# Kernel optimization log

Hardware: AMD Instinct MI355X
Metric: run time of the kernel (lower is better)

Reference implementation:

```python
import jax, jax.numpy as jnp
import numpy as np

DIM = 2048
NUM_HEADS = 16
HEAD_DIM = DIM // NUM_HEADS
HIDDEN = 4 * DIM
EPS = 1e-6


def rmsnorm(x, w):
    # Faithful to source: weight * (x * dim**-0.5 / sqrt(mean(x^2) + eps))
    scale = DIM ** -0.5
    norm = jnp.sqrt(jnp.mean(x * x, axis=-1, keepdims=True) + EPS)
    return w * (x * scale / norm)


def setup_inputs() -> dict:
    key = jax.random.key(0)
    ks = jax.random.split(key, 10)
    def init(k, shape, fan_in):
        return jax.random.normal(k, shape, dtype=jnp.float32) * (fan_in ** -0.5)
    return {
        "x": jax.random.normal(ks[0], (2, 2048, DIM), dtype=jnp.float32),
        "norm1_w": jnp.ones((DIM,), dtype=jnp.float32),
        "wq": init(ks[1], (DIM, DIM), DIM),
        "wk": init(ks[2], (HEAD_DIM, DIM), DIM),
        "wv": init(ks[3], (HEAD_DIM, DIM), DIM),
        "wo": init(ks[4], (DIM, DIM), DIM),
        "norm2_w": jnp.ones((DIM,), dtype=jnp.float32),
        "w1": init(ks[5], (HIDDEN, DIM), DIM),
        "w2": init(ks[6], (DIM, HIDDEN), HIDDEN),
        "w3": init(ks[7], (HIDDEN, DIM), DIM),
    }


def reference(x, norm1_w, wq, wk, wv, wo, norm2_w, w1, w2, w3):
    B, S, _ = x.shape
    # --- Multi-Query Attention (pre-norm) ---
    h = rmsnorm(x, norm1_w)
    q = h @ wq.T                                  # [B,S,D]
    k = h @ wk.T                                  # [B,S,hd] (shared across heads)
    v = h @ wv.T                                  # [B,S,hd]
    q = q.reshape(B, S, NUM_HEADS, HEAD_DIM)
    # scores: q @ k^T / sqrt(hd); k is broadcast (repeated) across heads
    scores = jnp.einsum('bshd,btd->bhst', q, k) / (HEAD_DIM ** 0.5)  # [B,H,S,S]
    probs = jax.nn.softmax(scores, axis=-1)
    attn = jnp.einsum('bhst,btd->bshd', probs, v).reshape(B, S, DIM)
    x = x + attn @ wo.T
    # --- SwiGLU FFN (pre-norm) ---
    h = rmsnorm(x, norm2_w)
    ffn = (jax.nn.silu(h @ w1.T) * (h @ w3.T)) @ w2.T
    return x + ffn
```

## Files before the change

kernel.cpp:

```cpp
#include <hip/hip_runtime.h>
#include <hip/hip_bf16.h>

typedef __attribute__((ext_vector_type(4))) float f32x4;
typedef __attribute__((ext_vector_type(8))) short s16x8;
typedef __attribute__((ext_vector_type(4))) short s16x4;
typedef __attribute__((ext_vector_type(2))) short s16x2;

#define MFMA_BF16 __builtin_amdgcn_mfma_f32_16x16x32_bf16

__device__ inline short f2bf(float f) {
  unsigned u = __float_as_uint(f);
  u = (u + 0x7FFFu + ((u >> 16) & 1u)) >> 16;
  return (short)u;
}
__device__ inline float bf2f(short s) {
  return __uint_as_float(((unsigned)(unsigned short)s) << 16);
}

#define DPPF(x, ctrl) __int_as_float(__builtin_amdgcn_update_dpp( \
    __float_as_int(x), __float_as_int(x), ctrl, 0xF, 0xF, false))
__device__ inline float rowmax16(float x) {
  x = fmaxf(x, DPPF(x, 0xB1));
  x = fmaxf(x, DPPF(x, 0x4E));
  x = fmaxf(x, DPPF(x, 0x124));
  x = fmaxf(x, DPPF(x, 0x128));
  return x;
}
__device__ inline float rowsum16(float x) {
  x += DPPF(x, 0xB1);
  x += DPPF(x, 0x4E);
  x += DPPF(x, 0x124);
  x += DPPF(x, 0x128);
  return x;
}

__device__ inline void supertile_map(int gx, int gy, int& bx, int& by) {
  int orig = blockIdx.y * gx + blockIdx.x;
  int x   = orig & 7;
  int lin = orig >> 3;
  int sw  = gx >> 3;
  int bg  = lin / (sw * 8);
  int rem = lin % (sw * 8);
  bx = x * sw + (rem >> 3);
  by = bg * 8 + (rem & 7);
}

__global__ __launch_bounds__(256) void cvt_kernel(
    const float* __restrict__ in, short* __restrict__ out, int n, float scale)
{
  int idx = (blockIdx.x * 256 + threadIdx.x) * 8;
  if (idx >= n) return;
  f32x4 a = *(const f32x4*)(in + idx);
  f32x4 b = *(const f32x4*)(in + idx + 4);
  s16x8 o;
  #pragma unroll
  for (int j = 0; j < 4; ++j) { o[j] = f2bf(a[j] * scale); o[4 + j] = f2bf(b[j] * scale); }
  *(s16x8*)(out + idx) = o;
}

__global__ __launch_bounds__(256) void rmsnorm_kernel(
    const float* __restrict__ x, const float* __restrict__ w, short* __restrict__ out)
{
  size_t row = blockIdx.x;
  const float* xr = x + row * 2048;
  int base = threadIdx.x * 8;
  f32x4 a = *(const f32x4*)(xr + base);
  f32x4 b = *(const f32x4*)(xr + base + 4);
  float ss = a[0]*a[0] + a[1]*a[1] + a[2]*a[2] + a[3]*a[3]
           + b[0]*b[0] + b[1]*b[1] + b[2]*b[2] + b[3]*b[3];
  #pragma unroll
  for (int off = 1; off < 64; off <<= 1) ss += __shfl_xor(ss, off, 64);
  __shared__ float red[4];
  if ((threadIdx.x & 63) == 0) red[threadIdx.x >> 6] = ss;
  __syncthreads();
  float tot = red[0] + red[1] + red[2] + red[3];
  float rn = rsqrtf(tot * (1.0f / 2048.0f) + 1e-6f) * 0.022097086912079608f;
  f32x4 wa = *(const f32x4*)(w + base);
  f32x4 wb = *(const f32x4*)(w + base + 4);
  s16x8 o;
  #pragma unroll
  for (int j = 0; j < 4; ++j) {
    o[j]     = f2bf(a[j] * wa[j] * rn);
    o[4 + j] = f2bf(b[j] * wb[j] * rn);
  }
  *(s16x8*)(out + row * 2048 + base) = o;
}

template <int MODE>
__global__ __launch_bounds__(256, 2) void gemm_bt_kernel(
    const short* __restrict__ A, const short* __restrict__ B,
    void* __restrict__ Cv, const float* __restrict__ resid,
    int M, int N, int K)
{
  __shared__ short As[128 * 32];
  __shared__ short Bs[128 * 32];
  int tid = threadIdx.x;
  int lane = tid & 63;
  int w = tid >> 6;
  int r = lane & 15, g = lane >> 4;
  int wr = w >> 1, wc = w & 1;
  size_t row0 = (size_t)blockIdx.y * 128;
  size_t col0 = (size_t)blockIdx.x * 128;

  f32x4 acc[4][4];
  #pragma unroll
  for (int i = 0; i < 4; ++i)
    #pragma unroll
    for (int j = 0; j < 4; ++j) acc[i][j] = (f32x4){0.f, 0.f, 0.f, 0.f};

  const short* Ablk = A + row0 * K;
  const short* Bblk = B + col0 * K;
  int arow = tid >> 2;
  int akk = (tid & 3) << 3;

  for (int k0 = 0; k0 < K; k0 += 32) {
    #pragma unroll
    for (int i = 0; i < 2; ++i) {
      int chunk = i * 256 + tid;
      int rr = i * 64 + arow;
      __builtin_amdgcn_global_load_lds(
          (const __attribute__((address_space(1))) unsigned int*)(Ablk + (size_t)rr * K + k0 + akk),
          (__attribute__((address_space(3))) unsigned int*)(&As[chunk * 8]), 16, 0, 0);
      __builtin_amdgcn_global_load_lds(
          (const __attribute__((address_space(1))) unsigned int*)(Bblk + (size_t)rr * K + k0 + akk),
          (__attribute__((address_space(3))) unsigned int*)(&Bs[chunk * 8]), 16, 0, 0);
    }
    __syncthreads();
    s16x8 af[4], bfr[4];
    #pragma unroll
    for (int mm = 0; mm < 4; ++mm)
      af[mm] = *(const s16x8*)(&As[(wr * 64 + mm * 16 + r) * 32 + g * 8]);
    #pragma unroll
    for (int nn = 0; nn < 4; ++nn)
      bfr[nn] = *(const s16x8*)(&Bs[(wc * 64 + nn * 16 + r) * 32 + g * 8]);
    #pragma unroll
    for (int mm = 0; mm < 4; ++mm)
      #pragma unroll
      for (int nn = 0; nn < 4; ++nn)
        acc[mm][nn] = MFMA_BF16(af[mm], bfr[nn], acc[mm][nn], 0, 0, 0);
    __syncthreads();
  }

  #pragma unroll
  for (int mm = 0; mm < 4; ++mm) {
    #pragma unroll
    for (int nn = 0; nn < 4; ++nn) {
      #pragma unroll
      for (int j = 0; j < 4; ++j) {
        size_t rr = row0 + wr * 64 + mm * 16 + g * 4 + j;
        size_t cc = col0 + wc * 64 + nn * 16 + r;
        size_t idx = rr * (size_t)N + cc;
        if constexpr (MODE == 0) {
          ((short*)Cv)[idx] = f2bf(acc[mm][nn][j]);
        } else {
          ((float*)Cv)[idx] = acc[mm][nn][j] + resid[idx];
        }
      }
    }
  }
}

#define STAGEA1(T)                                                             \
  _Pragma("unroll")                                                            \
  for (int i = 0; i < 4; ++i) {                                                \
    int lc = i * 256 + tid;                                                    \
    int rw = lc >> 3, ch = lc & 7;                                             \
    __builtin_amdgcn_global_load_lds(                                          \
        (const __attribute__((address_space(1))) unsigned int*)                \
            (Ablk + (size_t)rw * K + (T) * 64 + ((ch ^ (rw & 7)) << 3)),       \
        (__attribute__((address_space(3))) unsigned int*)                      \
            (&As[(T) & 1][lc * 8]), 16, 0, 0);                                 \
  }

#define STAGEB1(T)                                                             \
  _Pragma("unroll")                                                            \
  for (int i = 0; i < 4; ++i) {                                                \
    int lc = i * 256 + tid;                                                    \
    int rw = lc >> 3, ch = lc & 7;                                             \
    __builtin_amdgcn_global_load_lds(                                          \
        (const __attribute__((address_space(1))) unsigned int*)                \
            (Bblk + (size_t)rw * K + (T) * 64 + ((ch ^ (rw & 7)) << 3)),       \
        (__attribute__((address_space(3))) unsigned int*)                      \
            (&Bs[(T) & 1][lc * 8]), 16, 0, 0);                                 \
  }

#define LDK(KS, D)                                                             \
  _Pragma("unroll")                                                            \
  for (int mi = 0; mi < 4; ++mi) {                                             \
    int rowa = wr * 64 + mi * 16 + r;                                          \
    aR[mi] = *(const s16x8*)(&As[D][rowa * 64 + (((KS) * 4 + g) ^ (rowa & 7)) * 8]); \
  }                                                                            \
  _Pragma("unroll")                                                            \
  for (int ni = 0; ni < 4; ++ni) {                                             \
    int rowb = wc * 64 + ni * 16 + r;                                          \
    bR[ni] = *(const s16x8*)(&Bs[D][rowb * 64 + (((KS) * 4 + g) ^ (rowb & 7)) * 8]); \
  }

#define MF16A                                                                  \
  __builtin_amdgcn_s_setprio(1);                                               \
  _Pragma("unroll")                                                            \
  for (int mi = 0; mi < 4; ++mi)                                               \
    _Pragma("unroll")                                                          \
    for (int ni = 0; ni < 4; ++ni)                                             \
      acc[mi][ni] = MFMA_BF16(aR[mi], bR[ni], acc[mi][ni], 0, 0, 0);           \
  __builtin_amdgcn_s_setprio(0);

#define BAR __builtin_amdgcn_s_barrier()

template <int MODE>
__global__ __launch_bounds__(256, 2) void gemm128_kernel(
    const short* __restrict__ A, const short* __restrict__ B,
    void* __restrict__ Cv, const float* __restrict__ resid,
    int M, int N, int K)
{
  __shared__ short As[2][128 * 64];
  __shared__ short Bs[2][128 * 64];

  int tid = threadIdx.x;
  int lane = tid & 63;
  int w = tid >> 6;
  int r = lane & 15, g = lane >> 4;
  int wr = w >> 1, wc = w & 1;

  int bx, by;
  supertile_map(gridDim.x, gridDim.y, bx, by);
  size_t row0 = (size_t)by * 128;
  size_t col0 = (size_t)bx * 128;

  const short* Ablk = A + row0 * K;
  const short* Bblk = B + col0 * K;

  f32x4 acc[4][4];
  #pragma unroll
  for (int i = 0; i < 4; ++i)
    #pragma unroll
    for (int j = 0; j < 4; ++j) acc[i][j] = (f32x4){0.f, 0.f, 0.f, 0.f};

  s16x8 aR[4], bR[4];
  int NT = K >> 6;

  STAGEA1(0); STAGEB1(0);

  for (int t = 0; t < NT; ++t) {
    int d = t & 1;
    bool nl = (t < NT - 1);
    if (nl) {
      STAGEA1(t + 1); STAGEB1(t + 1);
      asm volatile("s_waitcnt vmcnt(8)" ::: "memory");
    } else {
      asm volatile("s_waitcnt vmcnt(0)" ::: "memory");
    }
    BAR;
    LDK(0, d);
    MF16A;
    LDK(1, d);
    MF16A;
    BAR;
  }

  #pragma unroll
  for (int mi = 0; mi < 4; ++mi) {
    #pragma unroll
    for (int ni = 0; ni < 4; ++ni) {
      #pragma unroll
      for (int j = 0; j < 4; ++j) {
        size_t rr = row0 + wr * 64 + mi * 16 + g * 4 + j;
        size_t cc = col0 + wc * 64 + ni * 16 + r;
        size_t idx = rr * (size_t)N + cc;
        if constexpr (MODE == 0) {
          ((short*)Cv)[idx] = f2bf(acc[mi][ni][j]);
        } else {
          ((float*)Cv)[idx] = acc[mi][ni][j] + resid[idx];
        }
      }
    }
  }
}

#define STG13(T, BASE, DST)                                                    \
  _Pragma("unroll")                                                            \
  for (int i = 0; i < 2; ++i) {                                                \
    int lc = i * 256 + tid;                                                    \
    int rw = lc >> 2, ch = lc & 3;                                             \
    __builtin_amdgcn_global_load_lds(                                          \
        (const __attribute__((address_space(1))) unsigned int*)                \
            (BASE + (size_t)rw * K + (T) * 32 + ((ch ^ ((rw >> 1) & 3)) << 3)),\
        (__attribute__((address_space(3))) unsigned int*)                      \
            (&DST[(T) & 1][lc * 8]), 16, 0, 0);                                \
  }

__global__ __launch_bounds__(256, 2) void gemm_w13_kernel(
    const short* __restrict__ A, const short* __restrict__ B1,
    const short* __restrict__ B3, short* __restrict__ C,
    int M, int N, int K)
{
  __shared__ short As[2][128 * 32];
  __shared__ short B1s[2][128 * 32];
  __shared__ short B3s[2][128 * 32];

  int tid = threadIdx.x;
  int lane = tid & 63;
  int w = tid >> 6;
  int r = lane & 15, g = lane >> 4;
  int wr = w >> 1, wc = w & 1;

  int bx, by;
  supertile_map(gridDim.x, gridDim.y, bx, by);
  size_t row0 = (size_t)by * 128;
  size_t col0 = (size_t)bx * 128;

  const short* Ablk  = A  + row0 * K;
  const short* B1blk = B1 + col0 * K;
  const short* B3blk = B3 + col0 * K;

  f32x4 acc1[4][4], acc3[4][4];
  #pragma unroll
  for (int i = 0; i < 4; ++i)
    #pragma unroll
    for (int j = 0; j < 4; ++j) {
      acc1[i][j] = (f32x4){0.f, 0.f, 0.f, 0.f};
      acc3[i][j] = (f32x4){0.f, 0.f, 0.f, 0.f};
    }

  s16x8 aR[4], b1R[4], b3R[4];
  int NT = K >> 5;

  STG13(0, Ablk, As); STG13(0, B1blk, B1s); STG13(0, B3blk, B3s);

  for (int t = 0; t < NT; ++t) {
    int d = t & 1;
    bool nl = (t < NT - 1);
    if (nl) {
      STG13(t + 1, Ablk, As); STG13(t + 1, B1blk, B1s); STG13(t + 1, B3blk, B3s);
      asm volatile("s_waitcnt vmcnt(6)" ::: "memory");
    } else {
      asm volatile("s_waitcnt vmcnt(0)" ::: "memory");
    }
    BAR;
    #pragma unroll
    for (int mi = 0; mi < 4; ++mi) {
      int rowa = wr * 64 + mi * 16 + r;
      aR[mi] = *(const s16x8*)(&As[d][rowa * 32 + ((g ^ ((rowa >> 1) & 3)) << 3)]);
    }
    #pragma unroll
    for (int ni = 0; ni < 4; ++ni) {
      int rowb = wc * 64 + ni * 16 + r;
      b1R[ni] = *(const s16x8*)(&B1s[d][rowb * 32 + ((g ^ ((rowb >> 1) & 3)) << 3)]);
      b3R[ni] = *(const s16x8*)(&B3s[d][rowb * 32 + ((g ^ ((rowb >> 1) & 3)) << 3)]);
    }
    __builtin_amdgcn_s_setprio(1);
    #pragma unroll
    for (int mi = 0; mi < 4; ++mi)
      #pragma unroll
      for (int ni = 0; ni < 4; ++ni) {
        acc1[mi][ni] = MFMA_BF16(aR[mi], b1R[ni], acc1[mi][ni], 0, 0, 0);
        acc3[mi][ni] = MFMA_BF16(aR[mi], b3R[ni], acc3[mi][ni], 0, 0, 0);
      }
    __builtin_amdgcn_s_setprio(0);
    BAR;
  }

  #pragma unroll
  for (int mi = 0; mi < 4; ++mi) {
    #pragma unroll
    for (int ni = 0; ni < 4; ++ni) {
      #pragma unroll
      for (int j = 0; j < 4; ++j) {
        size_t rr = row0 + wr * 64 + mi * 16 + g * 4 + j;
        size_t cc = col0 + wc * 64 + ni * 16 + r;
        float gv = acc1[mi][ni][j];
        float sg = gv / (1.0f + __expf(-gv));
        C[rr * (size_t)N + cc] = f2bf(sg * acc3[mi][ni][j]);
      }
    }
  }
}

__global__ __launch_bounds__(256) void transpose_v_kernel(
    const short* __restrict__ kv, short* __restrict__ vt)
{
  __shared__ short t[64][65];
  int b = blockIdx.z;
  int s0 = blockIdx.x * 64;
  int d0 = blockIdx.y * 64;
  int tid = threadIdx.x;
  #pragma unroll
  for (int i = 0; i < 16; ++i) {
    int e = i * 256 + tid;
    int sr = e >> 6, dc = e & 63;
    t[sr][dc] = kv[(size_t)(b * 2048 + s0 + sr) * 256 + 128 + d0 + dc];
  }
  __syncthreads();
  #pragma unroll
  for (int i = 0; i < 16; ++i) {
    int e = i * 256 + tid;
    int dr = e >> 6, sc = e & 63;
    vt[(size_t)b * 128 * 2048 + (size_t)(d0 + dr) * 2048 + s0 + sc] = t[sc][dr];
  }
}

__global__ __launch_bounds__(256, 2) void attn_kernel(
    const short* __restrict__ q, const short* __restrict__ kv,
    const short* __restrict__ vt, short* __restrict__ out)
{
  const int S = 2048;
  int tid = threadIdx.x;
  int w = tid >> 6;
  int lane = tid & 63;
  int r = lane & 15, g = lane >> 4;
  int h = blockIdx.y, b = blockIdx.z;
  int qrow0 = blockIdx.x * 128 + w * 32;

  __shared__ short Ks[2][4096];
  __shared__ short Vs[2][4096];
  __shared__ short Ps[4][32][40];

  const short* kvsrc = kv + (size_t)b * S * 256;
  const short* vsrc  = vt + (size_t)b * 128 * S;

  const short* qbase = q + ((size_t)(b * S + qrow0 + r)) * 2048 + h * 128;
  s16x8 qa[2][4];
  #pragma unroll
  for (int gq = 0; gq < 2; ++gq)
    #pragma unroll
    for (int dc = 0; dc < 4; ++dc)
      qa[gq][dc] = *(const s16x8*)(qbase + gq * 16 * 2048 + dc * 32 + g * 8);

  f32x4 o[2][8];
  #pragma unroll
  for (int gq = 0; gq < 2; ++gq)
    #pragma unroll
    for (int dt = 0; dt < 8; ++dt) o[gq][dt] = (f32x4){0.f, 0.f, 0.f, 0.f};
  float m[2][4], l[2][4];
  #pragma unroll
  for (int gq = 0; gq < 2; ++gq)
    #pragma unroll
    for (int j = 0; j < 4; ++j) { m[gq][j] = -1e30f; l[gq][j] = 0.f; }

#define STAGE(KVT, BSEL)                                                        \
  {                                                                             \
    int kv0s = (KVT) * 32;                                                      \
    _Pragma("unroll")                                                           \
    for (int i = 0; i < 2; ++i) {                                               \
      int c = w * 64 + lane + i * 256;                                          \
      int krow = c >> 4, kcp = c & 15;                                          \
      __builtin_amdgcn_global_load_lds(                                         \
          (const __attribute__((address_space(1))) unsigned int*)               \
              (kvsrc + (size_t)(kv0s + krow) * 256 + ((kcp ^ (krow & 7)) << 3)),\
          (__attribute__((address_space(3))) unsigned int*)(&Ks[BSEL][c * 8]),  \
          16, 0, 0);                                                            \
      int vrow = c >> 2, vcp = c & 3;                                           \
      __builtin_amdgcn_global_load_lds(                                         \
          (const __attribute__((address_space(1))) unsigned int*)               \
              (vsrc + (size_t)vrow * S + kv0s + ((vcp ^ (vrow & 3)) << 3)),     \
          (__attribute__((address_space(3))) unsigned int*)(&Vs[BSEL][c * 8]),  \
          16, 0, 0);                                                            \
    }                                                                           \
  }

  STAGE(0, 0);
  __syncthreads();

  for (int it = 0; it < 64; ++it) {
    int cur = it & 1;
    if (it < 63) STAGE(it + 1, cur ^ 1);

    s16x8 kc0[4], kc1[4], vb[8];
    #pragma unroll
    for (int dc = 0; dc < 4; ++dc) {
      kc0[dc] = *(const s16x8*)(&Ks[cur][r * 128 + (((dc * 4 + g) ^ (r & 7)) << 3)]);
      kc1[dc] = *(const s16x8*)(&Ks[cur][(16 + r) * 128 + (((dc * 4 + g) ^ (r & 7)) << 3)]);
    }
    #pragma unroll
    for (int dt = 0; dt < 8; ++dt)
      vb[dt] = *(const s16x8*)(&Vs[cur][(dt * 16 + r) * 32 + ((g ^ (r & 3)) << 3)]);

    f32x4 sc0[2], sc1[2];
    #pragma unroll
    for (int gq = 0; gq < 2; ++gq) { sc0[gq] = (f32x4){0.f,0.f,0.f,0.f}; sc1[gq] = (f32x4){0.f,0.f,0.f,0.f}; }
    __builtin_amdgcn_s_setprio(1);
    #pragma unroll
    for (int dc = 0; dc < 4; ++dc) {
      #pragma unroll
      for (int gq = 0; gq < 2; ++gq) {
        sc0[gq] = MFMA_BF16(qa[gq][dc], kc0[dc], sc0[gq], 0, 0, 0);
        sc1[gq] = MFMA_BF16(qa[gq][dc], kc1[dc], sc1[gq], 0, 0, 0);
      }
    }
    __builtin_amdgcn_s_setprio(0);

    float p0[2][4], p1[2][4];
    #pragma unroll
    for (int gq = 0; gq < 2; ++gq) {
      float mx[4];
      #pragma unroll
      for (int j = 0; j < 4; ++j) mx[j] = rowmax16(fmaxf(sc0[gq][j], sc1[gq][j]));
      bool nd = (mx[0] > m[gq][0] + 8.f) | (mx[1] > m[gq][1] + 8.f)
              | (mx[2] > m[gq][2] + 8.f) | (mx[3] > m[gq][3] + 8.f);
      if (__any(nd)) {
        #pragma unroll
        for (int j = 0; j < 4; ++j) {
          float mn = fmaxf(m[gq][j], mx[j]);
          float alpha = __expf(m[gq][j] - mn);
          m[gq][j] = mn;
          l[gq][j] *= alpha;
          #pragma unroll
          for (int dt = 0; dt < 8; ++dt) o[gq][dt][j] *= alpha;
        }
      }
      #pragma unroll
      for (int j = 0; j < 4; ++j) {
        p0[gq][j] = __expf(sc0[gq][j] - m[gq][j]);
        p1[gq][j] = __expf(sc1[gq][j] - m[gq][j]);
        l[gq][j] += p0[gq][j] + p1[gq][j];
      }
      #pragma unroll
      for (int j = 0; j < 4; ++j) {
        Ps[w][gq * 16 + g * 4 + j][r]      = f2bf(p0[gq][j]);
        Ps[w][gq * 16 + g * 4 + j][16 + r] = f2bf(p1[gq][j]);
      }
    }
    asm volatile("s_waitcnt lgkmcnt(0)" ::: "memory");
    __builtin_amdgcn_sched_barrier(0);
    s16x8 pa0 = *(const s16x8*)(&Ps[w][r][g * 8]);
    s16x8 pa1 = *(const s16x8*)(&Ps[w][16 + r][g * 8]);
    __builtin_amdgcn_s_setprio(1);
    #pragma unroll
    for (int dt = 0; dt < 8; ++dt) {
      o[0][dt] = MFMA_BF16(pa0, vb[dt], o[0][dt], 0, 0, 0);
      o[1][dt] = MFMA_BF16(pa1, vb[dt], o[1][dt], 0, 0, 0);
    }
    __builtin_amdgcn_s_setprio(0);
    __syncthreads();
  }

  #pragma unroll
  for (int gq = 0; gq < 2; ++gq) {
    float linv[4];
    #pragma unroll
    for (int j = 0; j < 4; ++j) linv[j] = 1.0f / rowsum16(l[gq][j]);
    short* ob = out + ((size_t)(b * S + qrow0 + gq * 16)) * 2048 + h * 128;
    #pragma unroll
    for (int dt = 0; dt < 8; ++dt)
      #pragma unroll
      for (int j = 0; j < 4; ++j)
        ob[(size_t)(g * 4 + j) * 2048 + dt * 16 + r] = f2bf(o[gq][dt][j] * linv[j]);
  }
#undef STAGE
}

extern "C" void kernel_launch(void* const* d_in, const int* in_sizes, int n_in,
                              void* d_out, int out_size, void* d_ws, size_t ws_size,
                              hipStream_t stream) {
  const float* x   = (const float*)d_in[0];
  const float* n1w = (const float*)d_in[1];
  const float* wq  = (const float*)d_in[2];
  const float* wk  = (const float*)d_in[3];
  const float* wv  = (const float*)d_in[4];
  const float* wo  = (const float*)d_in[5];
  const float* n2w = (const float*)d_in[6];
  const float* w1  = (const float*)d_in[7];
  const float* w2  = (const float*)d_in[8];
  const float* w3  = (const float*)d_in[9];
  float* out = (float*)d_out;
  char* ws = (char*)d_ws;
  const size_t MB = 1ull << 20;
  short* wqb  = (short*)(ws);
  short* wob  = (short*)(ws + 8 * MB);
  short* w1b  = (short*)(ws + 16 * MB);
  short* w2b  = (short*)(ws + 48 * MB);
  short* w3b  = (short*)(ws + 80 * MB);
  short* wkvb = (short*)(ws + 112 * MB);
  short* h1   = (short*)(ws + 113 * MB);
  short* gbuf = (short*)(ws + 129 * MB);
  short* qb   = (short*)(ws + 129 * MB);
  short* kvb  = (short*)(ws + 145 * MB);
  short* vtb  = (short*)(ws + 147 * MB);

  const float qscale = 0.08838834764831845f;
  cvt_kernel<<<2048, 256, 0, stream>>>(wq, wqb, 4194304, qscale);
  cvt_kernel<<<128,  256, 0, stream>>>(wk, wkvb, 262144, 1.0f);
  cvt_kernel<<<128,  256, 0, stream>>>(wv, wkvb + 262144, 262144, 1.0f);
  cvt_kernel<<<2048, 256, 0, stream>>>(wo, wob, 4194304, 1.0f);
  cvt_kernel<<<8192, 256, 0, stream>>>(w1, w1b, 16777216, 1.0f);
  cvt_kernel<<<8192, 256, 0, stream>>>(w2, w2b, 16777216, 1.0f);
  cvt_kernel<<<8192, 256, 0, stream>>>(w3, w3b, 16777216, 1.0f);

  rmsnorm_kernel<<<4096, 256, 0, stream>>>(x, n1w, h1);
  gemm128_kernel<0><<<dim3(16, 32), 256, 0, stream>>>(h1, wqb, qb, nullptr, 4096, 2048, 2048);
  gemm_bt_kernel<0><<<dim3(2, 32), 256, 0, stream>>>(h1, wkvb, kvb, nullptr, 4096, 256, 2048);
  transpose_v_kernel<<<dim3(32, 2, 2), 256, 0, stream>>>(kvb, vtb);
  attn_kernel<<<dim3(16, 16, 2), 256, 0, stream>>>(qb, kvb, vtb, h1);
  gemm128_kernel<1><<<dim3(16, 32), 256, 0, stream>>>(h1, wob, out, x, 4096, 2048, 2048);
  rmsnorm_kernel<<<4096, 256, 0, stream>>>(out, n2w, h1);
  gemm_w13_kernel<<<dim3(64, 32), 256, 0, stream>>>(h1, w1b, w3b, gbuf, 4096, 8192, 2048);
  gemm128_kernel<1><<<dim3(16, 32), 256, 0, stream>>>(gbuf, w2b, out, out, 4096, 2048, 8192);
}
```

Measured before the change: 807.3 us.

## Enlarge GEMM tile to 256x128 with BK=32 and 1x4 warp layout

Replaces the 128x128 tile GEMM (BK=64, 2x2 warps) with a 256x128 tile using BK=32, where each of the four waves owns 64 rows and the full 128 columns. Each wave now holds a 4x8 accumulator array, which doubles MFMA work per LDS fragment load and halves the grid. The goal is more data reuse per loaded byte and fewer redundant B-tile fetches. The cost is higher register pressure, which threatens occupancy of 2 blocks per SM. Only 256 blocks are launched for the 4096x2048 GEMMs, so CU utilization may drop.

```diff
diff --git a/kernel.cpp b/kernel.cpp
--- a/kernel.cpp
+++ b/kernel.cpp
@@ -160,112 +160,92 @@
   }
 }
 
-#define STAGEA1(T)                                                             \
+#define BAR __builtin_amdgcn_s_barrier()
+
+
+#define STG256(T, BASE, DST, NLOAD)                                            \
   _Pragma("unroll")                                                            \
-  for (int i = 0; i < 4; ++i) {                                                \
+  for (int i = 0; i < NLOAD; ++i) {                                            \
     int lc = i * 256 + tid;                                                    \
-    int rw = lc >> 3, ch = lc & 7;                                             \
+    int rw = lc >> 2, ch = lc & 3;                                             \
     __builtin_amdgcn_global_load_lds(                                          \
         (const __attribute__((address_space(1))) unsigned int*)                \
-            (Ablk + (size_t)rw * K + (T) * 64 + ((ch ^ (rw & 7)) << 3)),       \
+            (BASE + (size_t)rw * K + (T) * 32 + ((ch ^ ((rw >> 1) & 3)) << 3)),\
         (__attribute__((address_space(3))) unsigned int*)                      \
-            (&As[(T) & 1][lc * 8]), 16, 0, 0);                                 \
-  }
-
-#define STAGEB1(T)                                                             \
-  _Pragma("unroll")                                                            \
-  for (int i = 0; i < 4; ++i) {                                                \
-    int lc = i * 256 + tid;                                                    \
-    int rw = lc >> 3, ch = lc & 7;                                             \
-    __builtin_amdgcn_global_load_lds(                                          \
-        (const __attribute__((address_space(1))) unsigned int*)                \
-            (Bblk + (size_t)rw * K + (T) * 64 + ((ch ^ (rw & 7)) << 3)),       \
-        (__attribute__((address_space(3))) unsigned int*)                      \
-            (&Bs[(T) & 1][lc * 8]), 16, 0, 0);                                 \
-  }
-
-#define LDK(KS, D)                                                             \
-  _Pragma("unroll")                                                            \
-  for (int mi = 0; mi < 4; ++mi) {                                             \
-    int rowa = wr * 64 + mi * 16 + r;                                          \
-    aR[mi] = *(const s16x8*)(&As[D][rowa * 64 + (((KS) * 4 + g) ^ (rowa & 7)) * 8]); \
-  }                                                                            \
-  _Pragma("unroll")                                                            \
-  for (int ni = 0; ni < 4; ++ni) {                                             \
-    int rowb = wc * 64 + ni * 16 + r;                                          \
-    bR[ni] = *(const s16x8*)(&Bs[D][rowb * 64 + (((KS) * 4 + g) ^ (rowb & 7)) * 8]); \
-  }
-
-#define MF16A                                                                  \
-  __builtin_amdgcn_s_setprio(1);                                               \
-  _Pragma("unroll")                                                            \
-  for (int mi = 0; mi < 4; ++mi)                                               \
-    _Pragma("unroll")                                                          \
-    for (int ni = 0; ni < 4; ++ni)                                             \
-      acc[mi][ni] = MFMA_BF16(aR[mi], bR[ni], acc[mi][ni], 0, 0, 0);           \
-  __builtin_amdgcn_s_setprio(0);
-
-#define BAR __builtin_amdgcn_s_barrier()
+            (&DST[(T) & 1][lc * 8]), 16, 0, 0);                                \
+  }
 
 template <int MODE>
-__global__ __launch_bounds__(256, 2) void gemm128_kernel(
+__global__ __launch_bounds__(256, 2) void gemm256_kernel(
     const short* __restrict__ A, const short* __restrict__ B,
     void* __restrict__ Cv, const float* __restrict__ resid,
     int M, int N, int K)
 {
-  __shared__ short As[2][128 * 64];
-  __shared__ short Bs[2][128 * 64];
+  __shared__ short As[2][256 * 32];
+  __shared__ short Bs[2][128 * 32];
 
   int tid = threadIdx.x;
   int lane = tid & 63;
   int w = tid >> 6;
   int r = lane & 15, g = lane >> 4;
-  int wr = w >> 1, wc = w & 1;
 
   int bx, by;
   supertile_map(gridDim.x, gridDim.y, bx, by);
-  size_t row0 = (size_t)by * 128;
+  size_t row0 = (size_t)by * 256;
   size_t col0 = (size_t)bx * 128;
 
   const short* Ablk = A + row0 * K;
   const short* Bblk = B + col0 * K;
 
-  f32x4 acc[4][4];
+  f32x4 acc[4][8];
   #pragma unroll
   for (int i = 0; i < 4; ++i)
     #pragma unroll
-    for (int j = 0; j < 4; ++j) acc[i][j] = (f32x4){0.f, 0.f, 0.f, 0.f};
-
-  s16x8 aR[4], bR[4];
-  int NT = K >> 6;
-
-  STAGEA1(0); STAGEB1(0);
+    for (int j = 0; j < 8; ++j) acc[i][j] = (f32x4){0.f, 0.f, 0.f, 0.f};
+
+  s16x8 aR[4], bR[8];
+  int NT = K >> 5;
+
+  STG256(0, Ablk, As, 4); STG256(0, Bblk, Bs, 2);
 
   for (int t = 0; t < NT; ++t) {
     int d = t & 1;
     bool nl = (t < NT - 1);
     if (nl) {
-      STAGEA1(t + 1); STAGEB1(t + 1);
-      asm volatile("s_waitcnt vmcnt(8)" ::: "memory");
+      STG256(t + 1, Ablk, As, 4); STG256(t + 1, Bblk, Bs, 2);
+      asm volatile("s_waitcnt vmcnt(6)" ::: "memory");
     } else {
       asm volatile("s_waitcnt vmcnt(0)" ::: "memory");
     }
     BAR;
-    LDK(0, d);
-    MF16A;
-    LDK(1, d);
-    MF16A;
+    #pragma unroll
+    for (int mi = 0; mi < 4; ++mi) {
+      int rowa = w * 64 + mi * 16 + r;
+      aR[mi] = *(const s16x8*)(&As[d][rowa * 32 + ((g ^ ((rowa >> 1) & 3)) << 3)]);
+    }
+    #pragma unroll
+    for (int ni = 0; ni < 8; ++ni) {
+      int rowb = ni * 16 + r;
+      bR[ni] = *(const s16x8*)(&Bs[d][rowb * 32 + ((g ^ ((rowb >> 1) & 3)) << 3)]);
+    }
+    __builtin_amdgcn_s_setprio(1);
+    #pragma unroll
+    for (int mi = 0; mi < 4; ++mi)
+      #pragma unroll
+      for (int ni = 0; ni < 8; ++ni)
+        acc[mi][ni] = MFMA_BF16(aR[mi], bR[ni], acc[mi][ni], 0, 0, 0);
+    __builtin_amdgcn_s_setprio(0);
     BAR;
   }
 
   #pragma unroll
   for (int mi = 0; mi < 4; ++mi) {
     #pragma unroll
-    for (int ni = 0; ni < 4; ++ni) {
+    for (int ni = 0; ni < 8; ++ni) {
       #pragma unroll
       for (int j = 0; j < 4; ++j) {
-        size_t rr = row0 + wr * 64 + mi * 16 + g * 4 + j;
-        size_t cc = col0 + wc * 64 + ni * 16 + r;
+        size_t rr = row0 + w * 64 + mi * 16 + g * 4 + j;
+        size_t cc = col0 + ni * 16 + r;
         size_t idx = rr * (size_t)N + cc;
         if constexpr (MODE == 0) {
           ((short*)Cv)[idx] = f2bf(acc[mi][ni][j]);
@@ -587,12 +567,12 @@
   cvt_kernel<<<8192, 256, 0, stream>>>(w3, w3b, 16777216, 1.0f);
 
   rmsnorm_kernel<<<4096, 256, 0, stream>>>(x, n1w, h1);
-  gemm128_kernel<0><<<dim3(16, 32), 256, 0, stream>>>(h1, wqb, qb, nullptr, 4096, 2048, 2048);
+  gemm256_kernel<0><<<dim3(16, 16), 256, 0, stream>>>(h1, wqb, qb, nullptr, 4096, 2048, 2048);
   gemm_bt_kernel<0><<<dim3(2, 32), 256, 0, stream>>>(h1, wkvb, kvb, nullptr, 4096, 256, 2048);
   transpose_v_kernel<<<dim3(32, 2, 2), 256, 0, stream>>>(kvb, vtb);
   attn_kernel<<<dim3(16, 16, 2), 256, 0, stream>>>(qb, kvb, vtb, h1);
-  gemm128_kernel<1><<<dim3(16, 32), 256, 0, stream>>>(h1, wob, out, x, 4096, 2048, 2048);
+  gemm256_kernel<1><<<dim3(16, 16), 256, 0, stream>>>(h1, wob, out, x, 4096, 2048, 2048);
   rmsnorm_kernel<<<4096, 256, 0, stream>>>(out, n2w, h1);
   gemm_w13_kernel<<<dim3(64, 32), 256, 0, stream>>>(h1, w1b, w3b, gbuf, 4096, 8192, 2048);
-  gemm128_kernel<1><<<dim3(16, 32), 256, 0, stream>>>(gbuf, w2b, out, out, 4096, 2048, 8192);
-}
+  gemm256_kernel<1><<<dim3(16, 16), 256, 0, stream>>>(gbuf, w2b, out, out, 4096, 2048, 8192);
+}
```

Result: slower. 963.4 us (+19.3%).

## Triple-buffer w13 GEMM LDS pipeline and XCD-swizzle gemm128 block mapping

Applied to the files above, without the earlier changes.

The fused W1/W3 GEMM moves from double to triple buffering of its LDS tiles, prefetching two K-steps ahead with matching vmcnt waits, so global-load latency is hidden deeper behind MFMA work. The generic 128x128 GEMM swaps the supertile mapping for a simple modulo-8 swizzle that spreads consecutive workgroup IDs across chiplets. Triple buffering raises LDS use to 72KB per block, which may limit occupancy to two blocks per CU, and the new mapping gives up supertile L2 locality.

```diff
diff --git a/kernel.cpp b/kernel.cpp
--- a/kernel.cpp
+++ b/kernel.cpp
@@ -160,6 +160,8 @@
   }
 }
 
+#define BAR __builtin_amdgcn_s_barrier()
+
 #define STAGEA1(T)                                                             \
   _Pragma("unroll")                                                            \
   for (int i = 0; i < 4; ++i) {                                                \
@@ -205,8 +207,6 @@
       acc[mi][ni] = MFMA_BF16(aR[mi], bR[ni], acc[mi][ni], 0, 0, 0);           \
   __builtin_amdgcn_s_setprio(0);
 
-#define BAR __builtin_amdgcn_s_barrier()
-
 template <int MODE>
 __global__ __launch_bounds__(256, 2) void gemm128_kernel(
     const short* __restrict__ A, const short* __restrict__ B,
@@ -222,8 +222,10 @@
   int r = lane & 15, g = lane >> 4;
   int wr = w >> 1, wc = w & 1;
 
-  int bx, by;
-  supertile_map(gridDim.x, gridDim.y, bx, by);
+  int nwg = gridDim.x * gridDim.y;
+  int orig = blockIdx.y * gridDim.x + blockIdx.x;
+  int swz = (orig & 7) * (nwg >> 3) + (orig >> 3);
+  int bx = swz % gridDim.x, by = swz / gridDim.x;
   size_t row0 = (size_t)by * 128;
   size_t col0 = (size_t)bx * 128;
 
@@ -277,7 +279,8 @@
   }
 }
 
-#define STG13(T, BASE, DST)                                                    \
+
+#define STG13(T, D, BASE, DST)                                                 \
   _Pragma("unroll")                                                            \
   for (int i = 0; i < 2; ++i) {                                                \
     int lc = i * 256 + tid;                                                    \
@@ -286,7 +289,7 @@
         (const __attribute__((address_space(1))) unsigned int*)                \
             (BASE + (size_t)rw * K + (T) * 32 + ((ch ^ ((rw >> 1) & 3)) << 3)),\
         (__attribute__((address_space(3))) unsigned int*)                      \
-            (&DST[(T) & 1][lc * 8]), 16, 0, 0);                                \
+            (&DST[D][lc * 8]), 16, 0, 0);                                      \
   }
 
 __global__ __launch_bounds__(256, 2) void gemm_w13_kernel(
@@ -294,9 +297,9 @@
     const short* __restrict__ B3, short* __restrict__ C,
     int M, int N, int K)
 {
-  __shared__ short As[2][128 * 32];
-  __shared__ short B1s[2][128 * 32];
-  __shared__ short B3s[2][128 * 32];
+  __shared__ short As[3][128 * 32];
+  __shared__ short B1s[3][128 * 32];
+  __shared__ short B3s[3][128 * 32];
 
   int tid = threadIdx.x;
   int lane = tid & 63;
@@ -325,13 +328,17 @@
   s16x8 aR[4], b1R[4], b3R[4];
   int NT = K >> 5;
 
-  STG13(0, Ablk, As); STG13(0, B1blk, B1s); STG13(0, B3blk, B3s);
-
+  STG13(0, 0, Ablk, As); STG13(0, 0, B1blk, B1s); STG13(0, 0, B3blk, B3s);
+  STG13(1, 1, Ablk, As); STG13(1, 1, B1blk, B1s); STG13(1, 1, B3blk, B3s);
+
+  int bcur = 0, bstg = 2;
   for (int t = 0; t < NT; ++t) {
-    int d = t & 1;
-    bool nl = (t < NT - 1);
-    if (nl) {
-      STG13(t + 1, Ablk, As); STG13(t + 1, B1blk, B1s); STG13(t + 1, B3blk, B3s);
+    if (t + 2 < NT) {
+      STG13(t + 2, bstg, Ablk, As);
+      STG13(t + 2, bstg, B1blk, B1s);
+      STG13(t + 2, bstg, B3blk, B3s);
+      asm volatile("s_waitcnt vmcnt(12)" ::: "memory");
+    } else if (t + 1 < NT) {
       asm volatile("s_waitcnt vmcnt(6)" ::: "memory");
     } else {
       asm volatile("s_waitcnt vmcnt(0)" ::: "memory");
@@ -340,13 +347,13 @@
     #pragma unroll
     for (int mi = 0; mi < 4; ++mi) {
       int rowa = wr * 64 + mi * 16 + r;
-      aR[mi] = *(const s16x8*)(&As[d][rowa * 32 + ((g ^ ((rowa >> 1) & 3)) << 3)]);
+      aR[mi] = *(const s16x8*)(&As[bcur][rowa * 32 + ((g ^ ((rowa >> 1) & 3)) << 3)]);
     }
     #pragma unroll
     for (int ni = 0; ni < 4; ++ni) {
       int rowb = wc * 64 + ni * 16 + r;
-      b1R[ni] = *(const s16x8*)(&B1s[d][rowb * 32 + ((g ^ ((rowb >> 1) & 3)) << 3)]);
-      b3R[ni] = *(const s16x8*)(&B3s[d][rowb * 32 + ((g ^ ((rowb >> 1) & 3)) << 3)]);
+      b1R[ni] = *(const s16x8*)(&B1s[bcur][rowb * 32 + ((g ^ ((rowb >> 1) & 3)) << 3)]);
+      b3R[ni] = *(const s16x8*)(&B3s[bcur][rowb * 32 + ((g ^ ((rowb >> 1) & 3)) << 3)]);
     }
     __builtin_amdgcn_s_setprio(1);
     #pragma unroll
@@ -358,6 +365,8 @@
       }
     __builtin_amdgcn_s_setprio(0);
     BAR;
+    bcur = (bcur == 2) ? 0 : bcur + 1;
+    bstg = (bstg == 2) ? 0 : bstg + 1;
   }
 
   #pragma unroll
```

Result: faster. 787.9 us (-2.4%).
